# Kernel tuning notes

Measured on AMD Instinct MI355X. Metric: run time of the kernel, lower is better.

Reference implementation:

```python
import jax, jax.numpy as jnp
import numpy as np

N_BINS = 15


def _ece(logits, labels, n_bins=N_BINS):
    n, c, h, w = logits.shape
    # [n,c,h,w] -> [n*h*w, c]
    logits2d = jnp.transpose(logits, (0, 2, 3, 1)).reshape(-1, c)
    labels1d = labels.reshape(-1)
    softmaxes = jax.nn.softmax(logits2d, axis=1)
    confidences = jnp.max(softmaxes, axis=1)
    predictions = jnp.argmax(softmaxes, axis=1)
    correctness = (predictions == labels1d).astype(jnp.float32)

    # bin (lower, upper]: searchsorted(left) gives i+1 for conf in (b_i, b_{i+1}]
    boundaries = jnp.linspace(0.0, 1.0, n_bins + 1)
    bin_ids = jnp.clip(
        jnp.searchsorted(boundaries, confidences, side="left") - 1, 0, n_bins - 1
    )

    ones = jnp.ones_like(confidences)
    counts = jax.ops.segment_sum(ones, bin_ids, num_segments=n_bins)
    conf_sum = jax.ops.segment_sum(confidences, bin_ids, num_segments=n_bins)
    corr_sum = jax.ops.segment_sum(correctness, bin_ids, num_segments=n_bins)

    total = jnp.asarray(confidences.shape[0], jnp.float32)
    safe_counts = jnp.where(counts > 0, counts, 1.0)
    acc_in_bin = corr_sum / safe_counts
    avg_conf_in_bin = conf_sum / safe_counts
    prop_in_bin = counts / total
    gaps = jnp.where(counts > 0, jnp.abs(avg_conf_in_bin - acc_in_bin) * prop_in_bin, 0.0)
    return jnp.sum(gaps).reshape(1)


def setup_inputs() -> dict:
    key = jax.random.key(0)
    k1, k2 = jax.random.split(key)
    logits = jax.random.normal(k1, (8, 19, 512, 1024), dtype=jnp.float32)
    labels = jax.random.randint(k2, (8, 512, 1024), 0, 19, dtype=jnp.int64)
    return {"logits": logits, "labels": labels}


def reference(logits, labels):
    return _ece(logits, labels)
```

## Files before the change

### kernel.cpp

```cpp
#include <hip/hip_runtime.h>
#include <hip/hip_bf16.h>


constexpr int NBINS = 15;
constexpr int NC    = 19;
constexpr int REP   = 8;
constexpr int HWSH  = 19;

__global__ __launch_bounds__(256) void ece_partial_kernel(
    const float* __restrict__ logits,
    const int*   __restrict__ labels,
    double*       __restrict__ g_conf,
    unsigned int* __restrict__ g_cnt,
    unsigned int* __restrict__ g_corr,
    int P4)
{
    __shared__ float    s_conf[NBINS][REP];
    __shared__ unsigned s_cnt [NBINS][REP];
    __shared__ unsigned s_corr[NBINS][REP];

    const int t = threadIdx.x;
    for (int i = t; i < NBINS * REP; i += blockDim.x) {
        (&s_conf[0][0])[i] = 0.0f;
        (&s_cnt [0][0])[i] = 0u;
        (&s_corr[0][0])[i] = 0u;
    }
    __syncthreads();

    const int rep    = t & (REP - 1);
    const int HW     = 1 << HWSH;
    const int stride = gridDim.x * blockDim.x;

    for (int g = blockIdx.x * blockDim.x + t; g < P4; g += stride) {
        const int p   = g << 2;
        const int n   = p >> HWSH;
        const int rem = p & (HW - 1);
        const float* base = logits + (((size_t)(n * NC)) << HWSH) + rem;

        float v[NC][4];
        #pragma unroll
        for (int c = 0; c < NC; ++c) {
            const float4 x = *reinterpret_cast<const float4*>(base + ((size_t)c << HWSH));
            v[c][0] = x.x; v[c][1] = x.y; v[c][2] = x.z; v[c][3] = x.w;
        }
        const int4 lab = *reinterpret_cast<const int4*>(labels + p);
        const int labv[4] = { lab.x, lab.y, lab.z, lab.w };

        #pragma unroll
        for (int j = 0; j < 4; ++j) {
            float mx = v[0][j];
            int   am = 0;
            #pragma unroll
            for (int c = 1; c < NC; ++c) {
                if (v[c][j] > mx) { mx = v[c][j]; am = c; }
            }
            float s = 0.0f;
            #pragma unroll
            for (int c = 0; c < NC; ++c) s += __expf(v[c][j] - mx);
            const float conf = 1.0f / s;

            int b = (int)ceilf(conf * 15.0f) - 1;
            b = b < 0 ? 0 : (b > NBINS - 1 ? NBINS - 1 : b);

            atomicAdd(&s_cnt [b][rep], 1u);
            atomicAdd(&s_conf[b][rep], conf);
            if (am == labv[j]) atomicAdd(&s_corr[b][rep], 1u);
        }
    }
    __syncthreads();

    if (t < NBINS) {
        unsigned cnt = 0u, cor = 0u;
        float cf = 0.0f;
        #pragma unroll
        for (int r = 0; r < REP; ++r) {
            cnt += s_cnt [t][r];
            cor += s_corr[t][r];
            cf  += s_conf[t][r];
        }
        if (cnt) {
            atomicAdd(&g_cnt [t], cnt);
            atomicAdd(&g_corr[t], cor);
            atomicAdd(&g_conf[t], (double)cf);
        }
    }
}

__global__ void ece_final_kernel(const double* __restrict__ g_conf,
                                 const unsigned int* __restrict__ g_cnt,
                                 const unsigned int* __restrict__ g_corr,
                                 float* __restrict__ out, float total)
{
    if (threadIdx.x == 0 && blockIdx.x == 0) {
        double e = 0.0;
        for (int b = 0; b < NBINS; ++b) {
            const double c = (double)g_cnt[b];
            if (c > 0.0) {
                const double acc = (double)g_corr[b] / c;
                const double avg = g_conf[b] / c;
                e += fabs(avg - acc) * (c / (double)total);
            }
        }
        out[0] = (float)e;
    }
}

extern "C" void kernel_launch(void* const* d_in, const int* in_sizes, int n_in,
                              void* d_out, int out_size, void* d_ws, size_t ws_size,
                              hipStream_t stream) {
    const float* logits = (const float*)d_in[0];
    const int*   labels = (const int*)d_in[1];
    float*       out    = (float*)d_out;

    const int P  = in_sizes[1];
    const int P4 = P >> 2;

    double*       g_conf = (double*)d_ws;
    unsigned int* g_cnt  = (unsigned int*)((char*)d_ws + 128);
    unsigned int* g_corr = (unsigned int*)((char*)d_ws + 192);

    hipMemsetAsync(d_ws, 0, 256, stream);

    int blocks = (P4 + 255) / 256;
    if (blocks > 2048) blocks = 2048;
    ece_partial_kernel<<<blocks, 256, 0, stream>>>(logits, labels, g_conf, g_cnt, g_corr, P4);
    ece_final_kernel<<<1, 64, 0, stream>>>(g_conf, g_cnt, g_corr, out, (float)P);
}
```

Measured before the change: 81.22 us.

## Stream online softmax per channel and widen shared-memory bin replicas per lane

Replaces the load-all-19-channels-then-reduce pattern with an online max/sum softmax that consumes each channel's float4 as it arrives. This removes the 76-float register array and is meant to raise occupancy and memory-level parallelism in a bandwidth-bound kernel. Shared bin histograms are now replicated per wave lane (64 copies instead of 8) to cut LDS atomic contention. Count and correctness are packed into a single 32-bit atomic (high/low 16 bits), which saves one atomic per element but relies on per-block counts staying below 65536. The online update adds a serial dependency chain and a select per channel.

Measured after the change: 91.23 us. 1.12x slower.

```diff
diff --git a/kernel.cpp b/kernel.cpp
--- a/kernel.cpp
+++ b/kernel.cpp
@@ -4,8 +4,10 @@
 
 constexpr int NBINS = 15;
 constexpr int NC    = 19;
-constexpr int REP   = 8;
 constexpr int HWSH  = 19;
+
+typedef float f32x4 __attribute__((ext_vector_type(4)));
+typedef int   i32x4 __attribute__((ext_vector_type(4)));
 
 __global__ __launch_bounds__(256) void ece_partial_kernel(
     const float* __restrict__ logits,
@@ -15,72 +17,64 @@
     unsigned int* __restrict__ g_corr,
     int P4)
 {
-    __shared__ float    s_conf[NBINS][REP];
-    __shared__ unsigned s_cnt [NBINS][REP];
-    __shared__ unsigned s_corr[NBINS][REP];
+    __shared__ unsigned s_mc[NBINS * 64];
+    __shared__ float    s_cf[NBINS * 64];
 
     const int t = threadIdx.x;
-    for (int i = t; i < NBINS * REP; i += blockDim.x) {
-        (&s_conf[0][0])[i] = 0.0f;
-        (&s_cnt [0][0])[i] = 0u;
-        (&s_corr[0][0])[i] = 0u;
-    }
+    for (int i = t; i < NBINS * 64; i += 256) { s_mc[i] = 0u; s_cf[i] = 0.0f; }
     __syncthreads();
 
-    const int rep    = t & (REP - 1);
+    const int lane   = t & 63;
     const int HW     = 1 << HWSH;
-    const int stride = gridDim.x * blockDim.x;
+    const int stride = gridDim.x * 256;
 
-    for (int g = blockIdx.x * blockDim.x + t; g < P4; g += stride) {
+    for (int g = blockIdx.x * 256 + t; g < P4; g += stride) {
         const int p   = g << 2;
         const int n   = p >> HWSH;
         const int rem = p & (HW - 1);
         const float* base = logits + (((size_t)(n * NC)) << HWSH) + rem;
 
-        float v[NC][4];
+        const i32x4 lab = *reinterpret_cast<const i32x4*>(labels + p);
+
+        f32x4 x = *reinterpret_cast<const f32x4*>(base);
+        float m[4]  = { x[0], x[1], x[2], x[3] };
+        float s[4]  = { 1.0f, 1.0f, 1.0f, 1.0f };
+        int   am[4] = { 0, 0, 0, 0 };
+
         #pragma unroll
-        for (int c = 0; c < NC; ++c) {
-            const float4 x = *reinterpret_cast<const float4*>(base + ((size_t)c << HWSH));
-            v[c][0] = x.x; v[c][1] = x.y; v[c][2] = x.z; v[c][3] = x.w;
+        for (int c = 1; c < NC; ++c) {
+            const f32x4 v = *reinterpret_cast<const f32x4*>(base + ((size_t)c << HWSH));
+            #pragma unroll
+            for (int j = 0; j < 4; ++j) {
+                const float vj = v[j];
+                const bool  gt = vj > m[j];
+                const float e  = __expf(-fabsf(vj - m[j]));
+                s[j]  = gt ? s[j] * e + 1.0f : s[j] + e;
+                am[j] = gt ? c : am[j];
+                m[j]  = gt ? vj : m[j];
+            }
         }
-        const int4 lab = *reinterpret_cast<const int4*>(labels + p);
-        const int labv[4] = { lab.x, lab.y, lab.z, lab.w };
 
         #pragma unroll
         for (int j = 0; j < 4; ++j) {
-            float mx = v[0][j];
-            int   am = 0;
-            #pragma unroll
-            for (int c = 1; c < NC; ++c) {
-                if (v[c][j] > mx) { mx = v[c][j]; am = c; }
-            }
-            float s = 0.0f;
-            #pragma unroll
-            for (int c = 0; c < NC; ++c) s += __expf(v[c][j] - mx);
-            const float conf = 1.0f / s;
-
+            const float conf = 1.0f / s[j];
             int b = (int)ceilf(conf * 15.0f) - 1;
             b = b < 0 ? 0 : (b > NBINS - 1 ? NBINS - 1 : b);
-
-            atomicAdd(&s_cnt [b][rep], 1u);
-            atomicAdd(&s_conf[b][rep], conf);
-            if (am == labv[j]) atomicAdd(&s_corr[b][rep], 1u);
+            const int idx = b * 64 + lane;
+            atomicAdd(&s_mc[idx], 0x10000u | (unsigned)(am[j] == lab[j]));
+            atomicAdd(&s_cf[idx], conf);
         }
     }
     __syncthreads();
 
     if (t < NBINS) {
-        unsigned cnt = 0u, cor = 0u;
-        float cf = 0.0f;
-        #pragma unroll
-        for (int r = 0; r < REP; ++r) {
-            cnt += s_cnt [t][r];
-            cor += s_corr[t][r];
-            cf  += s_conf[t][r];
-        }
-        if (cnt) {
-            atomicAdd(&g_cnt [t], cnt);
-            atomicAdd(&g_corr[t], cor);
+        unsigned mc = 0u;
+        float    cf = 0.0f;
+        #pragma unroll 4
+        for (int r = 0; r < 64; ++r) { mc += s_mc[t * 64 + r]; cf += s_cf[t * 64 + r]; }
+        if (mc) {
+            atomicAdd(&g_cnt [t], mc >> 16);
+            atomicAdd(&g_corr[t], mc & 0xFFFFu);
             atomicAdd(&g_conf[t], (double)cf);
         }
     }
```
